# Kernel tuning notes

Measured on AMD Instinct MI355X. Metric: run time of the kernel, lower is better.

The kernel has to match this reference:

```python
import jax, jax.numpy as jnp
import numpy as np

D_MODEL = 1024
N_HEADS = 16
N_KV_HEADS = 4
D_K = D_MODEL // N_HEADS  # 64
GROUPS = N_HEADS // N_KV_HEADS
GATE_IN = 12
Q_SIZE = D_MODEL
KV_SIZE = N_KV_HEADS * D_K
QKV_SIZE = Q_SIZE + 2 * KV_SIZE
ROPE_BASE = 10000.0


def rms_norm(x, w):
    # torch nn.RMSNorm with eps=None -> finfo(dtype).eps
    eps = jnp.finfo(x.dtype).eps
    var = jnp.mean(x * x, axis=-1, keepdims=True)
    return x * jax.lax.rsqrt(var + eps) * w


def rope(x):
    # torchtune RotaryPositionalEmbeddings: interleaved pairs. x: [B,S,H,D]
    B, S, H, D = x.shape
    half = D // 2
    theta = 1.0 / (ROPE_BASE ** (jnp.arange(0, half, dtype=jnp.float32) * 2.0 / D))
    ang = jnp.arange(S, dtype=jnp.float32)[:, None] * theta[None, :]  # [S, half]
    cos = jnp.cos(ang)[None, :, None, :]
    sin = jnp.sin(ang)[None, :, None, :]
    xp = x.reshape(B, S, H, half, 2)
    x0, x1 = xp[..., 0], xp[..., 1]
    out = jnp.stack([x0 * cos - x1 * sin, x1 * cos + x0 * sin], axis=-1)
    return out.reshape(B, S, H, D).astype(x.dtype)


def setup_inputs() -> dict:
    key = jax.random.key(0)
    k1, k2, k3, k4, k5 = jax.random.split(key, 5)
    B, S = 2, 2048
    x = jax.random.normal(k1, (B, S, D_MODEL), dtype=jnp.float32)
    qkvo_proj = 0.02 * jax.random.normal(k2, (QKV_SIZE + D_MODEL, D_MODEL), dtype=jnp.float32)
    q_norm_w = jnp.ones((D_K,), dtype=jnp.float32) + 0.01 * jax.random.normal(k3, (D_K,), dtype=jnp.float32)
    k_norm_w = jnp.ones((D_K,), dtype=jnp.float32) + 0.01 * jax.random.normal(k4, (D_K,), dtype=jnp.float32)
    gate_w = 0.02 * jax.random.normal(k5, (N_HEADS, GATE_IN), dtype=jnp.float32)
    return {"x": x, "qkvo_proj": qkvo_proj, "q_norm_w": q_norm_w,
            "k_norm_w": k_norm_w, "gate_w": gate_w}


def reference(x, qkvo_proj, q_norm_w, k_norm_w, gate_w):
    B, S, _ = x.shape
    qkv = jnp.einsum('bsd,ed->bse', x, qkvo_proj[:QKV_SIZE])
    Q = qkv[..., :Q_SIZE].reshape(B, S, N_HEADS, D_K)
    K = qkv[..., Q_SIZE:Q_SIZE + KV_SIZE].reshape(B, S, N_KV_HEADS, D_K)
    V = qkv[..., Q_SIZE + KV_SIZE:].reshape(B, S, N_KV_HEADS, D_K)
    Q = rope(rms_norm(Q, q_norm_w))
    K = rope(rms_norm(K, k_norm_w))
    # GQA: repeat kv heads (repeat_interleave along head dim)
    K = jnp.repeat(K, GROUPS, axis=2)
    V = jnp.repeat(V, GROUPS, axis=2)
    scale = 1.0 / jnp.sqrt(jnp.float32(D_K))
    scores = jnp.einsum('bqhd,bkhd->bhqk', Q, K) * scale
    causal = jnp.tril(jnp.ones((S, S), dtype=bool))
    scores = jnp.where(causal[None, None], scores, jnp.float32(-jnp.inf))
    probs = jax.nn.softmax(scores, axis=-1)
    attn = jnp.einsum('bhqk,bkhd->bqhd', probs, V)  # [B,S,H,D_K]
    gate = jax.nn.sigmoid(jnp.einsum('bsg,hg->bsh', x[..., :GATE_IN], gate_w))
    attn = attn * gate[..., None]
    attn = attn.reshape(B, S, D_MODEL)
    return jnp.einsum('bsd,ed->bse', attn, qkvo_proj[QKV_SIZE:])
```

## Files before the change

kernel.cpp:

```cpp
#include <hip/hip_runtime.h>
#include <math.h>

typedef unsigned short u16;
typedef unsigned int u32;
typedef __bf16 bf16x8 __attribute__((ext_vector_type(8)));
typedef float f32x4 __attribute__((ext_vector_type(4)));
typedef unsigned short u16x8 __attribute__((ext_vector_type(8)));
typedef unsigned int u32x2 __attribute__((ext_vector_type(2)));

static __device__ __forceinline__ u16 f2bf(float f) {
  unsigned int u = __builtin_bit_cast(unsigned int, f);
  u = (u + 0x7FFFu + ((u >> 16) & 1u)) >> 16;
  return (u16)u;
}
static __device__ __forceinline__ float bf2f(u16 u) {
  unsigned int x = ((unsigned int)u) << 16;
  return __builtin_bit_cast(float, x);
}
static __device__ __forceinline__ u16 f2bfh(float f) {
  __bf16 b = (__bf16)f;
  return __builtin_bit_cast(u16, b);
}
static __device__ __forceinline__ void gll16(const u16* g, u16* l) {
  __builtin_amdgcn_global_load_lds((const __attribute__((address_space(1))) u32*)g,
                                   (__attribute__((address_space(3))) u32*)l, 16, 0, 0);
}

__global__ __launch_bounds__(256) void cvt2_bf16(const float* __restrict__ a, u16* __restrict__ da, int n4a,
                                                 const float* __restrict__ b, u16* __restrict__ db, int n4b) {
  int idx = blockIdx.x * 256 + threadIdx.x;
  const float* src; u16* dst; int i;
  if (idx < n4a) { src = a; dst = da; i = idx; }
  else { i = idx - n4a; if (i >= n4b) return; src = b; dst = db; }
  float4 v = ((const float4*)src)[i];
  ushort4 r;
  r.x = f2bf(v.x); r.y = f2bf(v.y); r.z = f2bf(v.z); r.w = f2bf(v.w);
  ((ushort4*)dst)[i] = r;
}

__global__ __launch_bounds__(256) void gemm_nt(const u16* __restrict__ A, const u16* __restrict__ B,
                                               float* __restrict__ C, int M, int N, int K) {
  __shared__ __align__(16) u16 sA[128 * 32];
  __shared__ __align__(16) u16 sB[128 * 32];
  const int tid = threadIdx.x;
  const int w = tid >> 6, lane = tid & 63, l15 = lane & 15;
  const int m0 = blockIdx.x * 128, n0 = blockIdx.y * 128;
  const int wm = (w >> 1) * 64, wn = (w & 1) * 64;

  f32x4 acc[4][4] = {};

  const int pb0 = w * 1024 + lane * 16;
  int srow[2], scol[2];
#pragma unroll
  for (int i = 0; i < 2; ++i) {
    int p = pb0 + i * 4096;
    int row = p >> 6, oo = p & 63;
    int ol = oo ^ (((row >> 1) & 3) << 4);
    srow[i] = row; scol[i] = ol >> 1;
  }
  int aoff[4], boff[4];
  const int kb = (lane >> 4) * 16;
#pragma unroll
  for (int m = 0; m < 4; ++m) {
    int r = wm + m * 16 + l15;
    aoff[m] = r * 64 + (kb ^ (((r >> 1) & 3) << 4));
  }
#pragma unroll
  for (int n = 0; n < 4; ++n) {
    int r = wn + n * 16 + l15;
    boff[n] = r * 64 + (kb ^ (((r >> 1) & 3) << 4));
  }

  for (int k0 = 0; k0 < K; k0 += 32) {
#pragma unroll
    for (int i = 0; i < 2; ++i) {
      int p = pb0 + i * 4096;
      gll16(A + (size_t)(m0 + srow[i]) * K + k0 + scol[i], (u16*)((char*)sA + p));
      gll16(B + (size_t)(n0 + srow[i]) * K + k0 + scol[i], (u16*)((char*)sB + p));
    }
    __syncthreads();
    bf16x8 af[4], bfr[4];
#pragma unroll
    for (int m = 0; m < 4; ++m) af[m] = *(const bf16x8*)((const char*)sA + aoff[m]);
#pragma unroll
    for (int n = 0; n < 4; ++n) bfr[n] = *(const bf16x8*)((const char*)sB + boff[n]);
#pragma unroll
    for (int m = 0; m < 4; ++m)
#pragma unroll
      for (int n = 0; n < 4; ++n)
        acc[m][n] = __builtin_amdgcn_mfma_f32_16x16x32_bf16(af[m], bfr[n], acc[m][n], 0, 0, 0);
    __syncthreads();
  }

#pragma unroll
  for (int m = 0; m < 4; ++m)
#pragma unroll
    for (int i = 0; i < 4; ++i) {
      int gr = m0 + wm + m * 16 + (lane >> 4) * 4 + i;
      float* crow = C + (size_t)gr * N + n0 + wn + l15;
#pragma unroll
      for (int n = 0; n < 4; ++n) crow[n * 16] = acc[m][n][i];
    }
}

#define QSCALE 0.18033688011112042f
__global__ __launch_bounds__(256) void norm_rope_gate(const float* __restrict__ qkv, const float* __restrict__ x,
                                                      const float* __restrict__ qw, const float* __restrict__ kw,
                                                      const float* __restrict__ gw,
                                                      u16* __restrict__ Q, u16* __restrict__ Kd,
                                                      u16* __restrict__ V, float* __restrict__ gate) {
  const int t = blockIdx.x * 4 + (threadIdx.x >> 6);
  const int lane = threadIdx.x & 63;
  const int b = t >> 11, s = t & 2047;
  const float* base = qkv + (size_t)t * 1536;
  const int ri = lane >> 1;
  float sn, cs;
  sincosf((float)s * expf(-(float)ri * (9.21034037198f / 32.0f)), &sn, &cs);
  const float qwl = qw[lane], kwl = kw[lane];

  for (int hh = 0; hh < 16; ++hh) {
    float v = base[hh * 64 + lane];
    float ss = v * v;
#pragma unroll
    for (int off = 32; off >= 1; off >>= 1) ss += __shfl_xor(ss, off);
    float r = rsqrtf(ss * (1.0f / 64.0f) + 1.1920929e-7f);
    float xn = v * r * qwl;
    float p = __shfl_xor(xn, 1);
    float outv = ((lane & 1) == 0) ? (xn * cs - p * sn) : (xn * cs + p * sn);
    Q[((size_t)(b * 16 + hh) * 2048 + s) * 64 + lane] = f2bf(outv * QSCALE);
  }
  for (int hh = 0; hh < 4; ++hh) {
    float v = base[1024 + hh * 64 + lane];
    float ss = v * v;
#pragma unroll
    for (int off = 32; off >= 1; off >>= 1) ss += __shfl_xor(ss, off);
    float r = rsqrtf(ss * (1.0f / 64.0f) + 1.1920929e-7f);
    float xn = v * r * kwl;
    float p = __shfl_xor(xn, 1);
    float outv = ((lane & 1) == 0) ? (xn * cs - p * sn) : (xn * cs + p * sn);
    Kd[((size_t)(b * 4 + hh) * 2048 + s) * 64 + lane] = f2bf(outv);
    V[((size_t)(b * 4 + hh) * 2048 + s) * 64 + lane] = f2bf(base[1280 + hh * 64 + lane]);
  }
  if (lane < 16) {
    float g = 0.f;
#pragma unroll
    for (int j = 0; j < 12; ++j) g += x[(size_t)t * 1024 + j] * gw[lane * 12 + j];
    gate[(size_t)t * 16 + lane] = 1.0f / (1.0f + __expf(-g));
  }
}

__global__ __launch_bounds__(256) void transpose_v64(const u16* __restrict__ V, u16* __restrict__ Vt) {
  __shared__ __align__(16) u16 tile[64][72];
  const int st = blockIdx.x, bh = blockIdx.y;
  const u16* src = V + ((size_t)bh * 2048 + st * 64) * 64;
  u16* dst = Vt + (size_t)bh * 64 * 2048 + st * 64;
  const int t = threadIdx.x;
  const int r = t >> 2, c0 = (t & 3) * 16;
#pragma unroll
  for (int j = 0; j < 2; ++j)
    *(u16x8*)&tile[r][c0 + j * 8] = *(const u16x8*)&src[(size_t)r * 64 + c0 + j * 8];
  __syncthreads();
  u16 tmp[16];
#pragma unroll
  for (int j = 0; j < 16; ++j) tmp[j] = tile[c0 + j][r];
#pragma unroll
  for (int j = 0; j < 2; ++j)
    *(u16x8*)&dst[(size_t)r * 2048 + c0 + j * 8] = *(const u16x8*)&tmp[j * 8];
}

__global__ __launch_bounds__(256) void attn_fwd_pair(const u16* __restrict__ Q, const u16* __restrict__ Kg,
                                                     const u16* __restrict__ Vt,
                                                     u16* __restrict__ accP, float* __restrict__ lP) {
  __shared__ __align__(16) u16 sK[2][64 * 64];
  __shared__ __align__(16) u16 sV[2][64 * 64];
  __shared__ __align__(16) u16 sP[4][16 * 64];

  const int tid = threadIdx.x;
  const int w = tid >> 6, lane = tid & 63;
  const int l15 = lane & 15, lg = lane >> 4;
  const int qiA = blockIdx.x;
  const int qiB = 31 - qiA;
  const int z = blockIdx.z;
  const int bh = blockIdx.y, b = bh >> 4, h = bh & 15, kvh = h >> 2;

  const u16* Qp = Q + (size_t)(b * 16 + h) * 2048 * 64;
  const u16* Kp = Kg + (size_t)(b * 4 + kvh) * 2048 * 64;
  const u16* Vp = Vt + (size_t)(b * 4 + kvh) * 64 * 2048;

  const int q0s[2] = {qiA * 64, qiB * 64};
  bf16x8 qa[2][2];
#pragma unroll
  for (int s = 0; s < 2; ++s) {
    const u16* qrow = Qp + (size_t)(q0s[s] + w * 16 + l15) * 64 + lg * 8;
    qa[s][0] = *(const bf16x8*)qrow;
    qa[s][1] = *(const bf16x8*)(qrow + 32);
  }

  f32x4 acc[2][4] = {};
  float l_s[2] = {0.f, 0.f};

  const int srw = tid >> 2;
  const int scb = (tid & 3) * 32;
  const int swzS = (srw & 7) << 4;
  const int st0 = srw * 128 + (scb ^ swzS);
  const int st1 = srw * 128 + ((scb + 16) ^ swzS);
  const u16* kgp = Kp + (size_t)srw * 64 + (tid & 3) * 16;
  const u16* vgp = Vp + (size_t)srw * 2048 + (tid & 3) * 16;

  const int swzF = (l15 & 7) << 4;
  const int fo0 = (lg * 16) ^ swzF;
  const int fo1 = (64 + lg * 16) ^ swzF;

  u16x8 kr0 = *(const u16x8*)(kgp + (size_t)z * 64 * 64), kr1 = *(const u16x8*)(kgp + (size_t)z * 64 * 64 + 8);
  u16x8 vr0 = *(const u16x8*)(vgp + z * 64),              vr1 = *(const u16x8*)(vgp + z * 64 + 8);
  *(u16x8*)((char*)sK[0] + st0) = kr0; *(u16x8*)((char*)sK[0] + st1) = kr1;
  *(u16x8*)((char*)sV[0] + st0) = vr0; *(u16x8*)((char*)sV[0] + st1) = vr1;
  __syncthreads();

  for (int t = z; t <= qiB; t += 2) {
    const int buf = (t >> 1) & 1;

    if (t + 2 <= qiB) {
      const u16* kg = kgp + (size_t)(t + 2) * 64 * 64;
      const u16* vg = vgp + (t + 2) * 64;
      kr0 = *(const u16x8*)kg; kr1 = *(const u16x8*)(kg + 8);
      vr0 = *(const u16x8*)vg; vr1 = *(const u16x8*)(vg + 8);
    }

    bf16x8 kf[4][2], vf[4][2];
#pragma unroll
    for (int ct = 0; ct < 4; ++ct) {
      const char* krow = (const char*)sK[buf] + (ct * 16 + l15) * 128;
      const char* vrow = (const char*)sV[buf] + (ct * 16 + l15) * 128;
      kf[ct][0] = *(const bf16x8*)(krow + fo0);
      kf[ct][1] = *(const bf16x8*)(krow + fo1);
      vf[ct][0] = *(const bf16x8*)(vrow + fo0);
      vf[ct][1] = *(const bf16x8*)(vrow + fo1);
    }

#pragma unroll
    for (int s = 0; s < 2; ++s) {
      if (s == 0 && t > qiA) continue;
      const int diag = s ? qiB : qiA;

      f32x4 st[4];
#pragma unroll
      for (int ct = 0; ct < 4; ++ct) {
        f32x4 s4 = {};
        s4 = __builtin_amdgcn_mfma_f32_16x16x32_bf16(kf[ct][0], qa[s][0], s4, 0, 0, 0);
        s4 = __builtin_amdgcn_mfma_f32_16x16x32_bf16(kf[ct][1], qa[s][1], s4, 0, 0, 0);
        st[ct] = s4;
      }

      if (t == diag) {
        const int ql = w * 16 + l15;
#pragma unroll
        for (int ct = 0; ct < 4; ++ct)
#pragma unroll
          for (int i = 0; i < 4; ++i)
            st[ct][i] = (ct * 16 + lg * 4 + i <= ql) ? st[ct][i] : -1e30f;
      }

      float ls = 0.f;
      const int swzP = (l15 & 7) << 4;
      char* prow = (char*)sP[w] + l15 * 128;
#pragma unroll
      for (int ct = 0; ct < 4; ++ct) {
        float p0 = exp2f(st[ct][0]), p1 = exp2f(st[ct][1]);
        float p2 = exp2f(st[ct][2]), p3 = exp2f(st[ct][3]);
        ls += (p0 + p1) + (p2 + p3);
        u32 lo = (u32)f2bfh(p0) | ((u32)f2bfh(p1) << 16);
        u32 hi = (u32)f2bfh(p2) | ((u32)f2bfh(p3) << 16);
        *(u32x2*)(prow + ((ct * 32 + lg * 8) ^ swzP)) = (u32x2){lo, hi};
      }
      l_s[s] += ls;

      bf16x8 pa0 = *(const bf16x8*)(prow + ((lg * 16) ^ swzP));
      bf16x8 pa1 = *(const bf16x8*)(prow + ((64 + lg * 16) ^ swzP));

#pragma unroll
      for (int n = 0; n < 4; ++n) {
        acc[s][n] = __builtin_amdgcn_mfma_f32_16x16x32_bf16(pa0, vf[n][0], acc[s][n], 0, 0, 0);
        acc[s][n] = __builtin_amdgcn_mfma_f32_16x16x32_bf16(pa1, vf[n][1], acc[s][n], 0, 0, 0);
      }
    }

    if (t + 2 <= qiB) {
      *(u16x8*)((char*)sK[buf ^ 1] + st0) = kr0; *(u16x8*)((char*)sK[buf ^ 1] + st1) = kr1;
      *(u16x8*)((char*)sV[buf ^ 1] + st0) = vr0; *(u16x8*)((char*)sV[buf ^ 1] + st1) = vr1;
    }
    __syncthreads();
  }

#pragma unroll
  for (int s = 0; s < 2; ++s) {
    float lv = l_s[s];
    lv += __shfl_xor(lv, 16);
    lv += __shfl_xor(lv, 32);
    if (lg == 0) {
      int qrow = q0s[s] + w * 16 + l15;
      lP[((size_t)z * 4096 + b * 2048 + qrow) * 16 + h] = lv;
    }
#pragma unroll
    for (int i = 0; i < 4; ++i) {
      int srowg = q0s[s] + w * 16 + lg * 4 + i;
      size_t rowbase = (size_t)z * 4096 + b * 2048 + srowg;
      u16* orow = accP + rowbase * 1024 + h * 64 + l15;
#pragma unroll
      for (int n = 0; n < 4; ++n) orow[n * 16] = f2bfh(acc[s][n][i]);
    }
  }
}

__global__ __launch_bounds__(256) void attn_combine(const u16* __restrict__ accP, const float* __restrict__ lP,
                                                    const float* __restrict__ gate, u16* __restrict__ attnh) {
  const size_t e = ((size_t)blockIdx.x * 256 + threadIdx.x) * 8;
  const int token = (int)(e >> 10);
  const int h = (int)((e >> 6) & 15);
  u16x8 a0 = *(const u16x8*)(accP + e);
  u16x8 a1 = *(const u16x8*)(accP + ((size_t)4096 << 10) + e);
  float l0 = lP[(size_t)token * 16 + h];
  float l1 = lP[(size_t)4096 * 16 + (size_t)token * 16 + h];
  float g = gate[(size_t)token * 16 + h] / (l0 + l1);
  u16x8 o;
#pragma unroll
  for (int j = 0; j < 8; ++j) o[j] = f2bfh((bf2f(a0[j]) + bf2f(a1[j])) * g);
  *(u16x8*)(attnh + e) = o;
}

extern "C" void kernel_launch(void* const* d_in, const int* in_sizes, int n_in,
                              void* d_out, int out_size, void* d_ws, size_t ws_size,
                              hipStream_t stream) {
  const float* x  = (const float*)d_in[0];
  const float* Wf = (const float*)d_in[1];
  const float* qw = (const float*)d_in[2];
  const float* kw = (const float*)d_in[3];
  const float* gw = (const float*)d_in[4];
  float* out = (float*)d_out;

  char* ws = (char*)d_ws;
  size_t off = 0;
  auto alloc = [&](size_t bytes) { void* p = ws + off; off += (bytes + 255) & ~(size_t)255; return p; };

  u16*   xb   = (u16*)alloc((size_t)4096 * 1024 * 2);
  u16*   wb   = (u16*)alloc((size_t)2560 * 1024 * 2);
  float* qkv  = (float*)alloc((size_t)4096 * 1536 * 4);
  u16*   Qb   = (u16*)alloc((size_t)2 * 16 * 2048 * 64 * 2);
  u16*   Kb   = (u16*)alloc((size_t)2 * 4 * 2048 * 64 * 2);
  u16*   Vb   = (u16*)alloc((size_t)2 * 4 * 2048 * 64 * 2);
  u16*   Vtb  = (u16*)alloc((size_t)2 * 4 * 2048 * 64 * 2);
  float* gate = (float*)alloc((size_t)2 * 2048 * 16 * 4);
  float* lP   = (float*)alloc((size_t)2 * 4096 * 16 * 4);
  u16* accP  = (u16*)qkv;
  u16* attnh = xb;

  cvt2_bf16<<<dim3(6656), dim3(256), 0, stream>>>(x, xb, 4096 * 1024 / 4, Wf, wb, 2560 * 1024 / 4);
  gemm_nt<<<dim3(32, 12), dim3(256), 0, stream>>>(xb, wb, qkv, 4096, 1536, 1024);
  norm_rope_gate<<<dim3(1024), dim3(256), 0, stream>>>(qkv, x, qw, kw, gw, Qb, Kb, Vb, gate);
  transpose_v64<<<dim3(32, 8), dim3(256), 0, stream>>>(Vb, Vtb);
  attn_fwd_pair<<<dim3(16, 32, 2), dim3(256), 0, stream>>>(Qb, Kb, Vtb, accP, lP);
  attn_combine<<<dim3(2048), dim3(256), 0, stream>>>(accP, lP, gate, attnh);
  gemm_nt<<<dim3(32, 8), dim3(256), 0, stream>>>(attnh, wb + (size_t)1536 * 1024, out, 4096, 1024, 1024);
}
```

Before: 135.2 us.

## Single-buffer K/V tiles and split QK/PV phases to raise occupancy

```diff
diff --git a/kernel.cpp b/kernel.cpp
--- a/kernel.cpp
+++ b/kernel.cpp
@@ -168,12 +168,12 @@
     *(u16x8*)&dst[(size_t)r * 2048 + c0 + j * 8] = *(const u16x8*)&tmp[j * 8];
 }
 
-__global__ __launch_bounds__(256) void attn_fwd_pair(const u16* __restrict__ Q, const u16* __restrict__ Kg,
-                                                     const u16* __restrict__ Vt,
-                                                     u16* __restrict__ accP, float* __restrict__ lP) {
-  __shared__ __align__(16) u16 sK[2][64 * 64];
-  __shared__ __align__(16) u16 sV[2][64 * 64];
-  __shared__ __align__(16) u16 sP[4][16 * 64];
+__global__ __launch_bounds__(256, 5) void attn_fwd_pair(const u16* __restrict__ Q, const u16* __restrict__ Kg,
+                                                        const u16* __restrict__ Vt,
+                                                        u16* __restrict__ accP, float* __restrict__ lP) {
+  __shared__ __align__(16) u16 sK[64 * 64];
+  __shared__ __align__(16) u16 sV[64 * 64];
+  __shared__ __align__(16) u16 sP[2][4][16 * 64];
 
   const int tid = threadIdx.x;
   const int w = tid >> 6, lane = tid & 63;
@@ -210,15 +210,18 @@
   const int swzF = (l15 & 7) << 4;
   const int fo0 = (lg * 16) ^ swzF;
   const int fo1 = (64 + lg * 16) ^ swzF;
+  const int swzP = swzF;
+  char* prow0 = (char*)sP[0][w] + l15 * 128;
+  char* prow1 = (char*)sP[1][w] + l15 * 128;
 
   u16x8 kr0 = *(const u16x8*)(kgp + (size_t)z * 64 * 64), kr1 = *(const u16x8*)(kgp + (size_t)z * 64 * 64 + 8);
   u16x8 vr0 = *(const u16x8*)(vgp + z * 64),              vr1 = *(const u16x8*)(vgp + z * 64 + 8);
-  *(u16x8*)((char*)sK[0] + st0) = kr0; *(u16x8*)((char*)sK[0] + st1) = kr1;
-  *(u16x8*)((char*)sV[0] + st0) = vr0; *(u16x8*)((char*)sV[0] + st1) = vr1;
-  __syncthreads();
 
   for (int t = z; t <= qiB; t += 2) {
-    const int buf = (t >> 1) & 1;
+    __syncthreads();
+    *(u16x8*)((char*)sK + st0) = kr0; *(u16x8*)((char*)sK + st1) = kr1;
+    *(u16x8*)((char*)sV + st0) = vr0; *(u16x8*)((char*)sV + st1) = vr1;
+    __syncthreads();
 
     if (t + 2 <= qiB) {
       const u16* kg = kgp + (size_t)(t + 2) * 64 * 64;
@@ -227,69 +230,75 @@
       vr0 = *(const u16x8*)vg; vr1 = *(const u16x8*)(vg + 8);
     }
 
-    bf16x8 kf[4][2], vf[4][2];
-#pragma unroll
-    for (int ct = 0; ct < 4; ++ct) {
-      const char* krow = (const char*)sK[buf] + (ct * 16 + l15) * 128;
-      const char* vrow = (const char*)sV[buf] + (ct * 16 + l15) * 128;
-      kf[ct][0] = *(const bf16x8*)(krow + fo0);
-      kf[ct][1] = *(const bf16x8*)(krow + fo1);
-      vf[ct][0] = *(const bf16x8*)(vrow + fo0);
-      vf[ct][1] = *(const bf16x8*)(vrow + fo1);
-    }
-
-#pragma unroll
-    for (int s = 0; s < 2; ++s) {
-      if (s == 0 && t > qiA) continue;
-      const int diag = s ? qiB : qiA;
-
-      f32x4 st[4];
+    {
+      bf16x8 kf[4][2];
 #pragma unroll
       for (int ct = 0; ct < 4; ++ct) {
-        f32x4 s4 = {};
-        s4 = __builtin_amdgcn_mfma_f32_16x16x32_bf16(kf[ct][0], qa[s][0], s4, 0, 0, 0);
-        s4 = __builtin_amdgcn_mfma_f32_16x16x32_bf16(kf[ct][1], qa[s][1], s4, 0, 0, 0);
-        st[ct] = s4;
+        const char* krow = (const char*)sK + (ct * 16 + l15) * 128;
+        kf[ct][0] = *(const bf16x8*)(krow + fo0);
+        kf[ct][1] = *(const bf16x8*)(krow + fo1);
       }
 
-      if (t == diag) {
-        const int ql = w * 16 + l15;
-#pragma unroll
-        for (int ct = 0; ct < 4; ++ct)
-#pragma unroll
-          for (int i = 0; i < 4; ++i)
-            st[ct][i] = (ct * 16 + lg * 4 + i <= ql) ? st[ct][i] : -1e30f;
+#pragma unroll
+      for (int s = 0; s < 2; ++s) {
+        if (s == 0 && t > qiA) continue;
+        const int diag = s ? qiB : qiA;
+
+        f32x4 st[4];
+#pragma unroll
+        for (int ct = 0; ct < 4; ++ct) {
+          f32x4 s4 = {};
+          s4 = __builtin_amdgcn_mfma_f32_16x16x32_bf16(kf[ct][0], qa[s][0], s4, 0, 0, 0);
+          s4 = __builtin_amdgcn_mfma_f32_16x16x32_bf16(kf[ct][1], qa[s][1], s4, 0, 0, 0);
+          st[ct] = s4;
+        }
+
+        if (t == diag) {
+          const int ql = w * 16 + l15;
+#pragma unroll
+          for (int ct = 0; ct < 4; ++ct)
+#pragma unroll
+            for (int i = 0; i < 4; ++i)
+              st[ct][i] = (ct * 16 + lg * 4 + i <= ql) ? st[ct][i] : -1e30f;
+        }
+
+        float ls = 0.f;
+        char* prow = s ? prow1 : prow0;
+#pragma unroll
+        for (int ct = 0; ct < 4; ++ct) {
+          float p0 = exp2f(st[ct][0]), p1 = exp2f(st[ct][1]);
+          float p2 = exp2f(st[ct][2]), p3 = exp2f(st[ct][3]);
+          ls += (p0 + p1) + (p2 + p3);
+          u32 lo = (u32)f2bfh(p0) | ((u32)f2bfh(p1) << 16);
+          u32 hi = (u32)f2bfh(p2) | ((u32)f2bfh(p3) << 16);
+          *(u32x2*)(prow + ((ct * 32 + lg * 8) ^ swzP)) = (u32x2){lo, hi};
+        }
+        l_s[s] += ls;
       }
-
-      float ls = 0.f;
-      const int swzP = (l15 & 7) << 4;
-      char* prow = (char*)sP[w] + l15 * 128;
+    }
+
+    {
+      bf16x8 vf[4][2];
 #pragma unroll
       for (int ct = 0; ct < 4; ++ct) {
-        float p0 = exp2f(st[ct][0]), p1 = exp2f(st[ct][1]);
-        float p2 = exp2f(st[ct][2]), p3 = exp2f(st[ct][3]);
-        ls += (p0 + p1) + (p2 + p3);
-        u32 lo = (u32)f2bfh(p0) | ((u32)f2bfh(p1) << 16);
-        u32 hi = (u32)f2bfh(p2) | ((u32)f2bfh(p3) << 16);
-        *(u32x2*)(prow + ((ct * 32 + lg * 8) ^ swzP)) = (u32x2){lo, hi};
+        const char* vrow = (const char*)sV + (ct * 16 + l15) * 128;
+        vf[ct][0] = *(const bf16x8*)(vrow + fo0);
+        vf[ct][1] = *(const bf16x8*)(vrow + fo1);
       }
-      l_s[s] += ls;
-
-      bf16x8 pa0 = *(const bf16x8*)(prow + ((lg * 16) ^ swzP));
-      bf16x8 pa1 = *(const bf16x8*)(prow + ((64 + lg * 16) ^ swzP));
-
-#pragma unroll
-      for (int n = 0; n < 4; ++n) {
-        acc[s][n] = __builtin_amdgcn_mfma_f32_16x16x32_bf16(pa0, vf[n][0], acc[s][n], 0, 0, 0);
-        acc[s][n] = __builtin_amdgcn_mfma_f32_16x16x32_bf16(pa1, vf[n][1], acc[s][n], 0, 0, 0);
+
+#pragma unroll
+      for (int s = 0; s < 2; ++s) {
+        if (s == 0 && t > qiA) continue;
+        const char* prow = s ? prow1 : prow0;
+        bf16x8 pa0 = *(const bf16x8*)(prow + ((lg * 16) ^ swzP));
+        bf16x8 pa1 = *(const bf16x8*)(prow + ((64 + lg * 16) ^ swzP));
+#pragma unroll
+        for (int n = 0; n < 4; ++n) {
+          acc[s][n] = __builtin_amdgcn_mfma_f32_16x16x32_bf16(pa0, vf[n][0], acc[s][n], 0, 0, 0);
+          acc[s][n] = __builtin_amdgcn_mfma_f32_16x16x32_bf16(pa1, vf[n][1], acc[s][n], 0, 0, 0);
+        }
       }
     }
-
-    if (t + 2 <= qiB) {
-      *(u16x8*)((char*)sK[buf ^ 1] + st0) = kr0; *(u16x8*)((char*)sK[buf ^ 1] + st1) = kr1;
-      *(u16x8*)((char*)sV[buf ^ 1] + st0) = vr0; *(u16x8*)((char*)sV[buf ^ 1] + st1) = vr1;
-    }
-    __syncthreads();
   }
 
 #pragma unroll
```

After: 217.2 us. +60.7%, slower.

## Process two query heads per attention block sharing K/V tiles, load via global_load_lds

Applied to the files above, without the earlier changes.

```diff
diff --git a/kernel.cpp b/kernel.cpp
--- a/kernel.cpp
+++ b/kernel.cpp
@@ -118,6 +118,7 @@
   sincosf((float)s * expf(-(float)ri * (9.21034037198f / 32.0f)), &sn, &cs);
   const float qwl = qw[lane], kwl = kw[lane];
 
+#pragma unroll 4
   for (int hh = 0; hh < 16; ++hh) {
     float v = base[hh * 64 + lane];
     float ss = v * v;
@@ -129,6 +130,7 @@
     float outv = ((lane & 1) == 0) ? (xn * cs - p * sn) : (xn * cs + p * sn);
     Q[((size_t)(b * 16 + hh) * 2048 + s) * 64 + lane] = f2bf(outv * QSCALE);
   }
+#pragma unroll
   for (int hh = 0; hh < 4; ++hh) {
     float v = base[1024 + hh * 64 + lane];
     float ss = v * v;
@@ -181,50 +183,58 @@
   const int qiA = blockIdx.x;
   const int qiB = 31 - qiA;
   const int z = blockIdx.z;
-  const int bh = blockIdx.y, b = bh >> 4, h = bh & 15, kvh = h >> 2;
-
-  const u16* Qp = Q + (size_t)(b * 16 + h) * 2048 * 64;
+  const int bhp = blockIdx.y, b = bhp >> 3, hp = bhp & 7, kvh = hp >> 1;
+  const int h0 = hp * 2;
+
   const u16* Kp = Kg + (size_t)(b * 4 + kvh) * 2048 * 64;
   const u16* Vp = Vt + (size_t)(b * 4 + kvh) * 64 * 2048;
 
   const int q0s[2] = {qiA * 64, qiB * 64};
-  bf16x8 qa[2][2];
-#pragma unroll
-  for (int s = 0; s < 2; ++s) {
-    const u16* qrow = Qp + (size_t)(q0s[s] + w * 16 + l15) * 64 + lg * 8;
+  bf16x8 qa[4][2];
+#pragma unroll
+  for (int s = 0; s < 4; ++s) {
+    const u16* qrow = Q + ((size_t)(b * 16 + h0 + (s & 1)) * 2048 + q0s[s >> 1] + w * 16 + l15) * 64 + lg * 8;
     qa[s][0] = *(const bf16x8*)qrow;
     qa[s][1] = *(const bf16x8*)(qrow + 32);
   }
 
-  f32x4 acc[2][4] = {};
-  float l_s[2] = {0.f, 0.f};
-
-  const int srw = tid >> 2;
-  const int scb = (tid & 3) * 32;
-  const int swzS = (srw & 7) << 4;
-  const int st0 = srw * 128 + (scb ^ swzS);
-  const int st1 = srw * 128 + ((scb + 16) ^ swzS);
-  const u16* kgp = Kp + (size_t)srw * 64 + (tid & 3) * 16;
-  const u16* vgp = Vp + (size_t)srw * 2048 + (tid & 3) * 16;
+  f32x4 acc[4][4] = {};
+  float l_s[4] = {0.f, 0.f, 0.f, 0.f};
+
+  int koff[2], voff[2], ldso[2];
+#pragma unroll
+  for (int i = 0; i < 2; ++i) {
+    int p = w * 1024 + i * 4096 + lane * 16;
+    int row = p >> 7, gcol = (p & 127) >> 4;
+    int sg = gcol ^ (row & 7);
+    ldso[i] = p;
+    koff[i] = row * 64 + sg * 8;
+    voff[i] = row * 2048 + sg * 8;
+  }
 
   const int swzF = (l15 & 7) << 4;
   const int fo0 = (lg * 16) ^ swzF;
   const int fo1 = (64 + lg * 16) ^ swzF;
-
-  u16x8 kr0 = *(const u16x8*)(kgp + (size_t)z * 64 * 64), kr1 = *(const u16x8*)(kgp + (size_t)z * 64 * 64 + 8);
-  u16x8 vr0 = *(const u16x8*)(vgp + z * 64),              vr1 = *(const u16x8*)(vgp + z * 64 + 8);
-  *(u16x8*)((char*)sK[0] + st0) = kr0; *(u16x8*)((char*)sK[0] + st1) = kr1;
-  *(u16x8*)((char*)sV[0] + st0) = vr0; *(u16x8*)((char*)sV[0] + st1) = vr1;
+  const int swzP = swzF;
+  char* prow = (char*)sP[w] + l15 * 128;
+
+#pragma unroll
+  for (int i = 0; i < 2; ++i) {
+    gll16(Kp + (size_t)z * 4096 + koff[i], (u16*)((char*)sK[0] + ldso[i]));
+    gll16(Vp + z * 64 + voff[i], (u16*)((char*)sV[0] + ldso[i]));
+  }
   __syncthreads();
 
-  for (int t = z; t <= qiB; t += 2) {
-    const int buf = (t >> 1) & 1;
+  int it = 0;
+  for (int t = z; t <= qiB; t += 2, ++it) {
+    const int buf = it & 1;
 
     if (t + 2 <= qiB) {
-      const u16* kg = kgp + (size_t)(t + 2) * 64 * 64;
-      const u16* vg = vgp + (t + 2) * 64;
-      kr0 = *(const u16x8*)kg; kr1 = *(const u16x8*)(kg + 8);
-      vr0 = *(const u16x8*)vg; vr1 = *(const u16x8*)(vg + 8);
+#pragma unroll
+      for (int i = 0; i < 2; ++i) {
+        gll16(Kp + (size_t)(t + 2) * 4096 + koff[i], (u16*)((char*)sK[buf ^ 1] + ldso[i]));
+        gll16(Vp + (t + 2) * 64 + voff[i], (u16*)((char*)sV[buf ^ 1] + ldso[i]));
+      }
     }
 
     bf16x8 kf[4][2], vf[4][2];
@@ -239,9 +249,9 @@
     }
 
 #pragma unroll
-    for (int s = 0; s < 2; ++s) {
-      if (s == 0 && t > qiA) continue;
-      const int diag = s ? qiB : qiA;
+    for (int s = 0; s < 4; ++s) {
+      if ((s >> 1) == 0 && t > qiA) continue;
+      const int diag = (s >> 1) ? qiB : qiA;
 
       f32x4 st[4];
 #pragma unroll
@@ -262,8 +272,6 @@
       }
 
       float ls = 0.f;
-      const int swzP = (l15 & 7) << 4;
-      char* prow = (char*)sP[w] + l15 * 128;
 #pragma unroll
       for (int ct = 0; ct < 4; ++ct) {
         float p0 = exp2f(st[ct][0]), p1 = exp2f(st[ct][1]);
@@ -285,27 +293,25 @@
       }
     }
 
-    if (t + 2 <= qiB) {
-      *(u16x8*)((char*)sK[buf ^ 1] + st0) = kr0; *(u16x8*)((char*)sK[buf ^ 1] + st1) = kr1;
-      *(u16x8*)((char*)sV[buf ^ 1] + st0) = vr0; *(u16x8*)((char*)sV[buf ^ 1] + st1) = vr1;
-    }
     __syncthreads();
   }
 
 #pragma unroll
-  for (int s = 0; s < 2; ++s) {
+  for (int s = 0; s < 4; ++s) {
+    const int hs = h0 + (s & 1);
+    const int q0 = q0s[s >> 1];
     float lv = l_s[s];
     lv += __shfl_xor(lv, 16);
     lv += __shfl_xor(lv, 32);
     if (lg == 0) {
-      int qrow = q0s[s] + w * 16 + l15;
-      lP[((size_t)z * 4096 + b * 2048 + qrow) * 16 + h] = lv;
+      int qrow = q0 + w * 16 + l15;
+      lP[((size_t)z * 4096 + b * 2048 + qrow) * 16 + hs] = lv;
     }
 #pragma unroll
     for (int i = 0; i < 4; ++i) {
-      int srowg = q0s[s] + w * 16 + lg * 4 + i;
+      int srowg = q0 + w * 16 + lg * 4 + i;
       size_t rowbase = (size_t)z * 4096 + b * 2048 + srowg;
-      u16* orow = accP + rowbase * 1024 + h * 64 + l15;
+      u16* orow = accP + rowbase * 1024 + hs * 64 + l15;
 #pragma unroll
       for (int n = 0; n < 4; ++n) orow[n * 16] = f2bfh(acc[s][n][i]);
     }
@@ -319,9 +325,9 @@
   const int h = (int)((e >> 6) & 15);
   u16x8 a0 = *(const u16x8*)(accP + e);
   u16x8 a1 = *(const u16x8*)(accP + ((size_t)4096 << 10) + e);
-  float l0 = lP[(size_t)token * 16 + h];
-  float l1 = lP[(size_t)4096 * 16 + (size_t)token * 16 + h];
-  float g = gate[(size_t)token * 16 + h] / (l0 + l1);
+  const size_t li = (size_t)token * 16 + h;
+  float l = lP[li] + lP[(size_t)4096 * 16 + li];
+  float g = gate[li] / l;
   u16x8 o;
 #pragma unroll
   for (int j = 0; j < 8; ++j) o[j] = f2bfh((bf2f(a0[j]) + bf2f(a1[j])) * g);
@@ -358,7 +364,7 @@
   gemm_nt<<<dim3(32, 12), dim3(256), 0, stream>>>(xb, wb, qkv, 4096, 1536, 1024);
   norm_rope_gate<<<dim3(1024), dim3(256), 0, stream>>>(qkv, x, qw, kw, gw, Qb, Kb, Vb, gate);
   transpose_v64<<<dim3(32, 8), dim3(256), 0, stream>>>(Vb, Vtb);
-  attn_fwd_pair<<<dim3(16, 32, 2), dim3(256), 0, stream>>>(Qb, Kb, Vtb, accP, lP);
+  attn_fwd_pair<<<dim3(16, 16, 2), dim3(256), 0, stream>>>(Qb, Kb, Vtb, accP, lP);
   attn_combine<<<dim3(2048), dim3(256), 0, stream>>>(accP, lP, gate, attnh);
   gemm_nt<<<dim3(32, 8), dim3(256), 0, stream>>>(attnh, wb + (size_t)1536 * 1024, out, 4096, 1024, 1024);
 }
```

Result: slower. 149.1 us (+10.3%).

## Fuse QK RMSNorm and RoPE into the QKV GEMM epilogue

Applied to the files above, without the earlier changes.

```diff
diff --git a/kernel.cpp b/kernel.cpp
--- a/kernel.cpp
+++ b/kernel.cpp
@@ -25,6 +25,8 @@
   __builtin_amdgcn_global_load_lds((const __attribute__((address_space(1))) u32*)g,
                                    (__attribute__((address_space(3))) u32*)l, 16, 0, 0);
 }
+
+#define QSCALE 0.18033688011112042f
 
 __global__ __launch_bounds__(256) void cvt2_bf16(const float* __restrict__ a, u16* __restrict__ da, int n4a,
                                                  const float* __restrict__ b, u16* __restrict__ db, int n4b) {
@@ -38,6 +40,14 @@
   ((ushort4*)dst)[i] = r;
 }
 
+__global__ __launch_bounds__(256) void rope_tab_k(float2* __restrict__ tab) {
+  int idx = blockIdx.x * 256 + threadIdx.x;
+  int s = idx >> 5, j = idx & 31;
+  float sn, cs;
+  sincosf((float)s * expf(-(float)j * (9.21034037198f / 32.0f)), &sn, &cs);
+  tab[idx] = make_float2(cs, sn);
+}
+
 __global__ __launch_bounds__(256) void gemm_nt(const u16* __restrict__ A, const u16* __restrict__ B,
                                                float* __restrict__ C, int M, int N, int K) {
   __shared__ __align__(16) u16 sA[128 * 32];
@@ -103,49 +113,108 @@
     }
 }
 
-#define QSCALE 0.18033688011112042f
-__global__ __launch_bounds__(256) void norm_rope_gate(const float* __restrict__ qkv, const float* __restrict__ x,
-                                                      const float* __restrict__ qw, const float* __restrict__ kw,
-                                                      const float* __restrict__ gw,
-                                                      u16* __restrict__ Q, u16* __restrict__ Kd,
-                                                      u16* __restrict__ V, float* __restrict__ gate) {
-  const int t = blockIdx.x * 4 + (threadIdx.x >> 6);
-  const int lane = threadIdx.x & 63;
-  const int b = t >> 11, s = t & 2047;
-  const float* base = qkv + (size_t)t * 1536;
-  const int ri = lane >> 1;
-  float sn, cs;
-  sincosf((float)s * expf(-(float)ri * (9.21034037198f / 32.0f)), &sn, &cs);
-  const float qwl = qw[lane], kwl = kw[lane];
-
-  for (int hh = 0; hh < 16; ++hh) {
-    float v = base[hh * 64 + lane];
-    float ss = v * v;
-#pragma unroll
-    for (int off = 32; off >= 1; off >>= 1) ss += __shfl_xor(ss, off);
-    float r = rsqrtf(ss * (1.0f / 64.0f) + 1.1920929e-7f);
-    float xn = v * r * qwl;
-    float p = __shfl_xor(xn, 1);
-    float outv = ((lane & 1) == 0) ? (xn * cs - p * sn) : (xn * cs + p * sn);
-    Q[((size_t)(b * 16 + hh) * 2048 + s) * 64 + lane] = f2bf(outv * QSCALE);
-  }
-  for (int hh = 0; hh < 4; ++hh) {
-    float v = base[1024 + hh * 64 + lane];
-    float ss = v * v;
-#pragma unroll
-    for (int off = 32; off >= 1; off >>= 1) ss += __shfl_xor(ss, off);
-    float r = rsqrtf(ss * (1.0f / 64.0f) + 1.1920929e-7f);
-    float xn = v * r * kwl;
-    float p = __shfl_xor(xn, 1);
-    float outv = ((lane & 1) == 0) ? (xn * cs - p * sn) : (xn * cs + p * sn);
-    Kd[((size_t)(b * 4 + hh) * 2048 + s) * 64 + lane] = f2bf(outv);
-    V[((size_t)(b * 4 + hh) * 2048 + s) * 64 + lane] = f2bf(base[1280 + hh * 64 + lane]);
-  }
-  if (lane < 16) {
-    float g = 0.f;
-#pragma unroll
-    for (int j = 0; j < 12; ++j) g += x[(size_t)t * 1024 + j] * gw[lane * 12 + j];
-    gate[(size_t)t * 16 + lane] = 1.0f / (1.0f + __expf(-g));
+__global__ __launch_bounds__(256) void gemm_qkv(const u16* __restrict__ A, const u16* __restrict__ B,
+                                                const float* __restrict__ qw, const float* __restrict__ kw,
+                                                const float2* __restrict__ tab,
+                                                u16* __restrict__ Qo, u16* __restrict__ Ko,
+                                                u16* __restrict__ Vo, int K) {
+  __shared__ __align__(16) u16 sA[128 * 32];
+  __shared__ __align__(16) u16 sB[128 * 32];
+  const int tid = threadIdx.x;
+  const int w = tid >> 6, lane = tid & 63, l15 = lane & 15, lg = lane >> 4;
+  const int m0 = blockIdx.x * 128, n0 = blockIdx.y * 128;
+  const int wm = (w >> 1) * 64, wn = (w & 1) * 64;
+
+  f32x4 acc[4][4] = {};
+
+  const int pb0 = w * 1024 + lane * 16;
+  int srow[2], scol[2];
+#pragma unroll
+  for (int i = 0; i < 2; ++i) {
+    int p = pb0 + i * 4096;
+    int row = p >> 6, oo = p & 63;
+    int ol = oo ^ (((row >> 1) & 3) << 4);
+    srow[i] = row; scol[i] = ol >> 1;
+  }
+  int aoff[4], boff[4];
+  const int kb = lg * 16;
+#pragma unroll
+  for (int m = 0; m < 4; ++m) {
+    int r = wm + m * 16 + l15;
+    aoff[m] = r * 64 + (kb ^ (((r >> 1) & 3) << 4));
+  }
+#pragma unroll
+  for (int n = 0; n < 4; ++n) {
+    int r = wn + n * 16 + l15;
+    boff[n] = r * 64 + (kb ^ (((r >> 1) & 3) << 4));
+  }
+
+  for (int k0 = 0; k0 < K; k0 += 32) {
+#pragma unroll
+    for (int i = 0; i < 2; ++i) {
+      int p = pb0 + i * 4096;
+      gll16(A + (size_t)(m0 + srow[i]) * K + k0 + scol[i], (u16*)((char*)sA + p));
+      gll16(B + (size_t)(n0 + srow[i]) * K + k0 + scol[i], (u16*)((char*)sB + p));
+    }
+    __syncthreads();
+    bf16x8 af[4], bfr[4];
+#pragma unroll
+    for (int m = 0; m < 4; ++m) af[m] = *(const bf16x8*)((const char*)sA + aoff[m]);
+#pragma unroll
+    for (int n = 0; n < 4; ++n) bfr[n] = *(const bf16x8*)((const char*)sB + boff[n]);
+#pragma unroll
+    for (int m = 0; m < 4; ++m)
+#pragma unroll
+      for (int n = 0; n < 4; ++n)
+        acc[m][n] = __builtin_amdgcn_mfma_f32_16x16x32_bf16(af[m], bfr[n], acc[m][n], 0, 0, 0);
+    __syncthreads();
+  }
+
+  const int he = (n0 + wn) >> 6;
+  if (he < 20) {
+    const float* wnorm = (he < 16) ? qw : kw;
+    const float oscale = (he < 16) ? QSCALE : 1.0f;
+    float wv[4];
+#pragma unroll
+    for (int n = 0; n < 4; ++n) wv[n] = wnorm[n * 16 + l15];
+    float2 tj[4];
+#pragma unroll
+    for (int m = 0; m < 4; ++m)
+#pragma unroll
+      for (int i = 0; i < 4; ++i) {
+        const int gr = m0 + wm + m * 16 + lg * 4 + i;
+        const int s = gr & 2047, bb = gr >> 11;
+        float ss = 0.f;
+#pragma unroll
+        for (int n = 0; n < 4; ++n) ss += acc[m][n][i] * acc[m][n][i];
+        ss += __shfl_xor(ss, 8); ss += __shfl_xor(ss, 4);
+        ss += __shfl_xor(ss, 2); ss += __shfl_xor(ss, 1);
+        const float r = rsqrtf(ss * (1.0f / 64.0f) + 1.1920929e-7f);
+#pragma unroll
+        for (int n = 0; n < 4; ++n) tj[n] = tab[s * 32 + n * 8 + (l15 >> 1)];
+        u16* orow = (he < 16)
+          ? Qo + ((size_t)(bb * 16 + he) * 2048 + s) * 64 + l15
+          : Ko + ((size_t)(bb * 4 + (he - 16)) * 2048 + s) * 64 + l15;
+#pragma unroll
+        for (int n = 0; n < 4; ++n) {
+          float xn = acc[m][n][i] * r * wv[n];
+          float p = __shfl_xor(xn, 1);
+          float outv = ((l15 & 1) == 0) ? (xn * tj[n].x - p * tj[n].y)
+                                        : (xn * tj[n].x + p * tj[n].y);
+          orow[n * 16] = f2bf(outv * oscale);
+        }
+      }
+  } else {
+#pragma unroll
+    for (int m = 0; m < 4; ++m)
+#pragma unroll
+      for (int i = 0; i < 4; ++i) {
+        const int gr = m0 + wm + m * 16 + lg * 4 + i;
+        const int s = gr & 2047, bb = gr >> 11;
+        u16* orow = Vo + ((size_t)(bb * 4 + (he - 20)) * 2048 + s) * 64 + l15;
+#pragma unroll
+        for (int n = 0; n < 4; ++n) orow[n * 16] = f2bf(acc[m][n][i]);
+      }
   }
 }
 
@@ -313,15 +382,19 @@
 }
 
 __global__ __launch_bounds__(256) void attn_combine(const u16* __restrict__ accP, const float* __restrict__ lP,
-                                                    const float* __restrict__ gate, u16* __restrict__ attnh) {
+                                                    const float* __restrict__ x, const float* __restrict__ gw,
+                                                    u16* __restrict__ attnh) {
   const size_t e = ((size_t)blockIdx.x * 256 + threadIdx.x) * 8;
   const int token = (int)(e >> 10);
   const int h = (int)((e >> 6) & 15);
   u16x8 a0 = *(const u16x8*)(accP + e);
   u16x8 a1 = *(const u16x8*)(accP + ((size_t)4096 << 10) + e);
-  float l0 = lP[(size_t)token * 16 + h];
-  float l1 = lP[(size_t)4096 * 16 + (size_t)token * 16 + h];
-  float g = gate[(size_t)token * 16 + h] / (l0 + l1);
+  const size_t li = (size_t)token * 16 + h;
+  float l = lP[li] + lP[(size_t)4096 * 16 + li];
+  float gd = 0.f;
+#pragma unroll
+  for (int j = 0; j < 12; ++j) gd += x[(size_t)token * 1024 + j] * gw[h * 12 + j];
+  float g = (1.0f / (1.0f + __expf(-gd))) / l;
   u16x8 o;
 #pragma unroll
   for (int j = 0; j < 8; ++j) o[j] = f2bfh((bf2f(a0[j]) + bf2f(a1[j])) * g);
@@ -342,23 +415,22 @@
   size_t off = 0;
   auto alloc = [&](size_t bytes) { void* p = ws + off; off += (bytes + 255) & ~(size_t)255; return p; };
 
-  u16*   xb   = (u16*)alloc((size_t)4096 * 1024 * 2);
-  u16*   wb   = (u16*)alloc((size_t)2560 * 1024 * 2);
-  float* qkv  = (float*)alloc((size_t)4096 * 1536 * 4);
-  u16*   Qb   = (u16*)alloc((size_t)2 * 16 * 2048 * 64 * 2);
-  u16*   Kb   = (u16*)alloc((size_t)2 * 4 * 2048 * 64 * 2);
-  u16*   Vb   = (u16*)alloc((size_t)2 * 4 * 2048 * 64 * 2);
-  u16*   Vtb  = (u16*)alloc((size_t)2 * 4 * 2048 * 64 * 2);
-  float* gate = (float*)alloc((size_t)2 * 2048 * 16 * 4);
-  float* lP   = (float*)alloc((size_t)2 * 4096 * 16 * 4);
-  u16* accP  = (u16*)qkv;
+  u16*    xb   = (u16*)alloc((size_t)4096 * 1024 * 2);
+  u16*    wb   = (u16*)alloc((size_t)2560 * 1024 * 2);
+  float2* tab  = (float2*)alloc((size_t)2048 * 32 * 8);
+  u16*    Qb   = (u16*)alloc((size_t)2 * 16 * 2048 * 64 * 2);
+  u16*    Kb   = (u16*)alloc((size_t)2 * 4 * 2048 * 64 * 2);
+  u16*    Vb   = (u16*)alloc((size_t)2 * 4 * 2048 * 64 * 2);
+  u16*    Vtb  = (u16*)alloc((size_t)2 * 4 * 2048 * 64 * 2);
+  float*  lP   = (float*)alloc((size_t)2 * 4096 * 16 * 4);
+  u16*    accP = (u16*)alloc((size_t)2 * 4096 * 1024 * 2);
   u16* attnh = xb;
 
   cvt2_bf16<<<dim3(6656), dim3(256), 0, stream>>>(x, xb, 4096 * 1024 / 4, Wf, wb, 2560 * 1024 / 4);
-  gemm_nt<<<dim3(32, 12), dim3(256), 0, stream>>>(xb, wb, qkv, 4096, 1536, 1024);
-  norm_rope_gate<<<dim3(1024), dim3(256), 0, stream>>>(qkv, x, qw, kw, gw, Qb, Kb, Vb, gate);
+  rope_tab_k<<<dim3(256), dim3(256), 0, stream>>>(tab);
+  gemm_qkv<<<dim3(32, 12), dim3(256), 0, stream>>>(xb, wb, qw, kw, tab, Qb, Kb, Vb, 1024);
   transpose_v64<<<dim3(32, 8), dim3(256), 0, stream>>>(Vb, Vtb);
   attn_fwd_pair<<<dim3(16, 32, 2), dim3(256), 0, stream>>>(Qb, Kb, Vtb, accP, lP);
-  attn_combine<<<dim3(2048), dim3(256), 0, stream>>>(accP, lP, gate, attnh);
+  attn_combine<<<dim3(2048), dim3(256), 0, stream>>>(accP, lP, x, gw, attnh);
   gemm_nt<<<dim3(32, 8), dim3(256), 0, stream>>>(attnh, wb + (size_t)1536 * 1024, out, 4096, 1024, 1024);
 }
```

Result: faster. 129.8 us (-3.9%).
